# Kernel optimization log

Measured on AMD Instinct MI355X. Metric: run time of the kernel, lower is better.

Reference implementation:

```python
import jax, jax.numpy as jnp
import numpy as np

EPS = 1e-5
H = 96  # spatial size (scaled from 256 to fit memory budget)


def _conv3x3(x, w):
    return jax.lax.conv_general_dilated(x, w, (1, 1), ((1, 1), (1, 1)),
                                        dimension_numbers=('NCHW', 'OIHW', 'NCHW'))


def _conv1x1(x, w, b=None):
    y = jax.lax.conv_general_dilated(x, w, (1, 1), 'VALID',
                                     dimension_numbers=('NCHW', 'OIHW', 'NCHW'))
    if b is not None:
        y = y + b[None, :, None, None]
    return y


def _ln(x, w, b):
    # LayerNorm over (C,H,W) with per-element affine, torch semantics
    m = jnp.mean(x, axis=(1, 2, 3), keepdims=True)
    v = jnp.mean(jnp.square(x - m), axis=(1, 2, 3), keepdims=True)
    return (x - m) * jax.lax.rsqrt(v + EPS) * w[None] + b[None]


def setup_inputs() -> dict:
    key = jax.random.key(0)
    ks = iter(jax.random.split(key, 32))
    s = 0.05
    d = {}
    d['x'] = jax.random.normal(next(ks), (1, 237, H, H), dtype=jnp.float32)
    d['conv1_w'] = jax.random.normal(next(ks), (96, 237, 3, 3), jnp.float32) * s
    d['ln1_w'] = jnp.ones((96, H, H), jnp.float32)
    d['ln1_b'] = jnp.zeros((96, H, H), jnp.float32)
    d['conv2_w'] = jax.random.normal(next(ks), (48, 96, 3, 3), jnp.float32) * s
    d['ln2_w'] = jnp.ones((48, H, H), jnp.float32)
    d['ln2_b'] = jnp.zeros((48, H, H), jnp.float32)
    d['conv3_w'] = jax.random.normal(next(ks), (48, 48, 3, 3), jnp.float32) * s
    d['ln3_w'] = jnp.ones((48, H, H), jnp.float32)
    d['ln3_b'] = jnp.zeros((48, H, H), jnp.float32)
    d['conv4_w'] = jax.random.normal(next(ks), (17, 48, 3, 3), jnp.float32) * s
    d['ln4_w'] = jnp.ones((17, H, H), jnp.float32)
    d['ln4_b'] = jnp.zeros((17, H, H), jnp.float32)
    d['cam_gamma'] = jax.random.normal(next(ks), (1,), jnp.float32) * 0.1
    # PAM (dim_reduse=1 -> 17->17 q/k/v 1x1 convs, bias=True)
    d['q_w'] = jax.random.normal(next(ks), (17, 17, 1, 1), jnp.float32) * s
    d['q_b'] = jnp.zeros((17,), jnp.float32)
    d['k_w'] = jax.random.normal(next(ks), (17, 17, 1, 1), jnp.float32) * s
    d['k_b'] = jnp.zeros((17,), jnp.float32)
    d['v_w'] = jax.random.normal(next(ks), (17, 17, 1, 1), jnp.float32) * s
    d['v_b'] = jnp.zeros((17,), jnp.float32)
    d['pam_gamma'] = jax.random.normal(next(ks), (1,), jnp.float32) * 0.1
    d['conv5_w'] = jax.random.normal(next(ks), (17, 17, 1, 1), jnp.float32) * s
    d['ln5_w'] = jnp.ones((17, H, H), jnp.float32)
    d['ln5_b'] = jnp.zeros((17, H, H), jnp.float32)
    d['conv6_w'] = jax.random.normal(next(ks), (17, 17, 1, 1), jnp.float32) * s
    return d


def reference(x, conv1_w, ln1_w, ln1_b, conv2_w, ln2_w, ln2_b,
              conv3_w, ln3_w, ln3_b, conv4_w, ln4_w, ln4_b,
              cam_gamma, q_w, q_b, k_w, k_b, v_w, v_b, pam_gamma,
              conv5_w, ln5_w, ln5_b, conv6_w):
    # backbone: (conv3x3 -> LN -> ReLU) x4
    h = jax.nn.relu(_ln(_conv3x3(x, conv1_w), ln1_w, ln1_b))
    h = jax.nn.relu(_ln(_conv3x3(h, conv2_w), ln2_w, ln2_b))
    h = jax.nn.relu(_ln(_conv3x3(h, conv3_w), ln3_w, ln3_b))
    h = jax.nn.relu(_ln(_conv3x3(h, conv4_w), ln4_w, ln4_b))

    B, C, Hh, Ww = h.shape
    N = Hh * Ww
    hf = h.reshape(B, C, N)

    # CAM: channel attention, [B,C,C]
    e = jnp.einsum('bcn,bdn->bcd', hf, hf)
    e_new = jnp.max(e, axis=-1, keepdims=True) - e
    a_c = jax.nn.softmax(e_new, axis=-1)
    cam = (a_c @ hf).reshape(B, C, Hh, Ww) * cam_gamma

    # PAM: position attention, [B,N,N] (the huge memory-bound matrix)
    q = _conv1x1(h, q_w, q_b).reshape(B, -1, N)   # [B,Cq,N]
    k = _conv1x1(h, k_w, k_b).reshape(B, -1, N)   # [B,Cq,N]
    v = _conv1x1(h, v_w, v_b).reshape(B, C, N)    # [B,C,N]
    energy = jnp.einsum('bcn,bcm->bnm', q, k)      # [B,N,N]
    a_p = jax.nn.softmax(energy, axis=-1)
    pam = jnp.einsum('bcm,bnm->bcn', v, a_p).reshape(B, C, Hh, Ww) * pam_gamma

    y = cam + pam + h
    y = jax.nn.relu(_ln(_conv1x1(y, conv5_w), ln5_w, ln5_b))
    y = _conv1x1(y, conv6_w)
    return y
```

## Files before the change

kernel.cpp:

```cpp
#include <hip/hip_runtime.h>
#include <math.h>

#define HH 96
#define NPIX 9216
#define KSPLIT 32
#define KEYS_PER_SPLIT 288
#define TK 96


__global__ __launch_bounds__(64) void zero_stats_kernel(float* stats) {
    if (threadIdx.x < 16) stats[threadIdx.x] = 0.f;
}

__global__ __launch_bounds__(256) void conv3x3_kernel(
        const float* __restrict__ in, const float* __restrict__ w,
        float* __restrict__ out, int Cin, int Cout) {
    extern __shared__ float smem[];
    float* wl   = smem;
    float* tile = smem + 4 * Cin * 9;

    const int tx = threadIdx.x, ty = threadIdx.y;
    const int tid = ty * 16 + tx;
    const int x0 = blockIdx.x * 16, y0 = blockIdx.y * 16;
    const int co_base = blockIdx.z * 4;
    const int nco = min(4, Cout - co_base);
    const int wcount = nco * Cin * 9;

    for (int i = tid; i < wcount; i += 256)
        wl[i] = w[co_base * Cin * 9 + i];

    float acc[4] = {0.f, 0.f, 0.f, 0.f};

    for (int ci = 0; ci < Cin; ++ci) {
        __syncthreads();
        for (int i = tid; i < 324; i += 256) {
            int r = i / 18, c = i - r * 18;
            int gy = y0 + r - 1, gx = x0 + c - 1;
            float v = 0.f;
            if (gy >= 0 && gy < HH && gx >= 0 && gx < HH)
                v = in[ci * NPIX + gy * HH + gx];
            tile[i] = v;
        }
        __syncthreads();

        float v[9];
        #pragma unroll
        for (int dy = 0; dy < 3; ++dy)
            #pragma unroll
            for (int dx = 0; dx < 3; ++dx)
                v[dy * 3 + dx] = tile[(ty + dy) * 18 + tx + dx];

        #pragma unroll
        for (int j = 0; j < 4; ++j) {
            const float* wp = wl + j * Cin * 9 + ci * 9;
            float a = acc[j];
            #pragma unroll
            for (int kk = 0; kk < 9; ++kk) a += wp[kk] * v[kk];
            acc[j] = a;
        }
    }

    const int oy = y0 + ty, ox = x0 + tx;
    #pragma unroll
    for (int j = 0; j < 4; ++j)
        if (j < nco)
            out[(co_base + j) * NPIX + oy * HH + ox] = acc[j];
}

__global__ __launch_bounds__(256) void ln_reduce_kernel(
        const float* __restrict__ x, int n, float* stats) {
    float s = 0.f, s2 = 0.f;
    for (int i = blockIdx.x * 256 + threadIdx.x; i < n; i += gridDim.x * 256) {
        float v = x[i];
        s += v; s2 += v * v;
    }
    #pragma unroll
    for (int off = 32; off > 0; off >>= 1) {
        s  += __shfl_down(s,  off);
        s2 += __shfl_down(s2, off);
    }
    __shared__ float ls[4], ls2[4];
    int wid = threadIdx.x >> 6;
    if ((threadIdx.x & 63) == 0) { ls[wid] = s; ls2[wid] = s2; }
    __syncthreads();
    if (threadIdx.x == 0) {
        float a = ls[0] + ls[1] + ls[2] + ls[3];
        float b = ls2[0] + ls2[1] + ls2[2] + ls2[3];
        atomicAdd(&stats[0], a);
        atomicAdd(&stats[1], b);
    }
}

__global__ __launch_bounds__(256) void ln_apply_relu_kernel(
        float* __restrict__ x, const float* __restrict__ w,
        const float* __restrict__ b, const float* __restrict__ stats,
        int n, float inv_n) {
    int i = blockIdx.x * 256 + threadIdx.x;
    if (i >= n) return;
    float m   = stats[0] * inv_n;
    float var = stats[1] * inv_n - m * m;
    float inv = rsqrtf(var + 1e-5f);
    float t = (x[i] - m) * inv * w[i] + b[i];
    x[i] = t > 0.f ? t : 0.f;
}

__global__ __launch_bounds__(256) void qkv_kernel(
        const float* __restrict__ h,
        const float* __restrict__ qw, const float* __restrict__ qb,
        const float* __restrict__ kw, const float* __restrict__ kb,
        const float* __restrict__ vw, const float* __restrict__ vb,
        float* __restrict__ q, float* __restrict__ k, float* __restrict__ v) {
    int n = blockIdx.x * 256 + threadIdx.x;
    if (n >= NPIX) return;
    float hv[17];
    #pragma unroll
    for (int c = 0; c < 17; ++c) hv[c] = h[c * NPIX + n];
    #pragma unroll
    for (int co = 0; co < 17; ++co) {
        float sq = qb[co], sk = kb[co], sv = vb[co];
        #pragma unroll
        for (int ci = 0; ci < 17; ++ci) {
            float hh = hv[ci];
            sq += qw[co * 17 + ci] * hh;
            sk += kw[co * 17 + ci] * hh;
            sv += vw[co * 17 + ci] * hh;
        }
        q[co * NPIX + n] = sq;
        k[co * NPIX + n] = sk;
        v[co * NPIX + n] = sv;
    }
}

__global__ __launch_bounds__(256) void cam_e_kernel(const float* __restrict__ h, float* e) {
    int c = blockIdx.x / 17, d = blockIdx.x - c * 17;
    float s = 0.f;
    for (int i = threadIdx.x; i < NPIX; i += 256)
        s += h[c * NPIX + i] * h[d * NPIX + i];
    #pragma unroll
    for (int off = 32; off > 0; off >>= 1) s += __shfl_down(s, off);
    __shared__ float red[4];
    int wid = threadIdx.x >> 6;
    if ((threadIdx.x & 63) == 0) red[wid] = s;
    __syncthreads();
    if (threadIdx.x == 0) e[blockIdx.x] = red[0] + red[1] + red[2] + red[3];
}

__global__ __launch_bounds__(64) void cam_softmax_kernel(const float* __restrict__ e,
                                                         float* __restrict__ a) {
    int c = threadIdx.x;
    if (c >= 17) return;
    float rmax = -1e30f, rmin = 1e30f;
    for (int d = 0; d < 17; ++d) {
        float v = e[c * 17 + d];
        rmax = fmaxf(rmax, v);
        rmin = fminf(rmin, v);
    }
    float mm = rmax - rmin;
    float p[17], sum = 0.f;
    for (int d = 0; d < 17; ++d) {
        p[d] = __expf((rmax - e[c * 17 + d]) - mm);
        sum += p[d];
    }
    float inv = 1.f / sum;
    for (int d = 0; d < 17; ++d) a[c * 17 + d] = p[d] * inv;
}

__global__ __launch_bounds__(256) void pam_flash_kernel(
        const float* __restrict__ q, const float* __restrict__ k,
        const float* __restrict__ v,
        float* __restrict__ m_part, float* __restrict__ l_part,
        float* __restrict__ o_part) {
    __shared__ float kt[17][TK];
    __shared__ float vt[17][TK];
    const int qi = blockIdx.x * 256 + threadIdx.x;
    const int sp = blockIdx.y;
    const int k0 = sp * KEYS_PER_SPLIT;

    float qr[17];
    #pragma unroll
    for (int c = 0; c < 17; ++c) qr[c] = q[c * NPIX + qi];

    float mr = -1e30f, lr = 0.f;
    float orr[17];
    #pragma unroll
    for (int c = 0; c < 17; ++c) orr[c] = 0.f;

    for (int t = 0; t < KEYS_PER_SPLIT / TK; ++t) {
        __syncthreads();
        for (int i = threadIdx.x; i < 17 * TK; i += 256) {
            int c = i / TK, mi = i - c * TK;
            kt[c][mi] = k[c * NPIX + k0 + t * TK + mi];
            vt[c][mi] = v[c * NPIX + k0 + t * TK + mi];
        }
        __syncthreads();
        for (int mm = 0; mm < TK; ++mm) {
            float s0 = 0.f, s1 = 0.f;
            #pragma unroll
            for (int c = 0; c < 16; c += 2) {
                s0 += qr[c]     * kt[c][mm];
                s1 += qr[c + 1] * kt[c + 1][mm];
            }
            float s = s0 + s1 + qr[16] * kt[16][mm];
            if (s > mr + 8.f) {
                float sc = __expf(mr - s);
                lr *= sc;
                #pragma unroll
                for (int c = 0; c < 17; ++c) orr[c] *= sc;
                mr = s;
            }
            float p = __expf(s - mr);
            lr += p;
            #pragma unroll
            for (int c = 0; c < 17; ++c) orr[c] += p * vt[c][mm];
        }
    }

    m_part[sp * NPIX + qi] = mr;
    l_part[sp * NPIX + qi] = lr;
    #pragma unroll
    for (int c = 0; c < 17; ++c)
        o_part[(sp * 17 + c) * NPIX + qi] = orr[c];
}

__global__ __launch_bounds__(256) void pam_merge_kernel(
        const float* __restrict__ m_part, const float* __restrict__ l_part,
        const float* __restrict__ o_part, const float* __restrict__ gamma,
        float* __restrict__ pam) {
    const int qi = blockIdx.x * 256 + threadIdx.x;
    float M = -1e30f;
    #pragma unroll
    for (int s = 0; s < KSPLIT; ++s) M = fmaxf(M, m_part[s * NPIX + qi]);
    float wsc[KSPLIT];
    float L = 0.f;
    #pragma unroll
    for (int s = 0; s < KSPLIT; ++s) {
        float wv = __expf(m_part[s * NPIX + qi] - M);
        wsc[s] = wv;
        L += wv * l_part[s * NPIX + qi];
    }
    float invL = gamma[0] / L;
    for (int c = 0; c < 17; ++c) {
        float acc = 0.f;
        #pragma unroll
        for (int s = 0; s < KSPLIT; ++s)
            acc += wsc[s] * o_part[(s * 17 + c) * NPIX + qi];
        pam[c * NPIX + qi] = acc * invL;
    }
}

__global__ __launch_bounds__(256) void y_combine_kernel(
        const float* __restrict__ h, const float* __restrict__ a,
        const float* __restrict__ cam_gamma, const float* __restrict__ pam,
        float* __restrict__ y) {
    int idx = blockIdx.x * 256 + threadIdx.x;
    if (idx >= 17 * NPIX) return;
    int c = idx / NPIX, n = idx - c * NPIX;
    float s = 0.f;
    #pragma unroll
    for (int d = 0; d < 17; ++d) s += a[c * 17 + d] * h[d * NPIX + n];
    y[idx] = cam_gamma[0] * s + pam[idx] + h[idx];
}

__global__ __launch_bounds__(256) void conv1x1_17_kernel(
        const float* __restrict__ in, const float* __restrict__ w,
        float* __restrict__ out) {
    int idx = blockIdx.x * 256 + threadIdx.x;
    if (idx >= 17 * NPIX) return;
    int c = idx / NPIX, n = idx - c * NPIX;
    float s = 0.f;
    #pragma unroll
    for (int ci = 0; ci < 17; ++ci) s += w[c * 17 + ci] * in[ci * NPIX + n];
    out[idx] = s;
}


extern "C" void kernel_launch(void* const* d_in, const int* in_sizes, int n_in,
                              void* d_out, int out_size, void* d_ws, size_t ws_size,
                              hipStream_t stream) {
    const float* x       = (const float*)d_in[0];
    const float* conv1_w = (const float*)d_in[1];
    const float* ln1_w   = (const float*)d_in[2];
    const float* ln1_b   = (const float*)d_in[3];
    const float* conv2_w = (const float*)d_in[4];
    const float* ln2_w   = (const float*)d_in[5];
    const float* ln2_b   = (const float*)d_in[6];
    const float* conv3_w = (const float*)d_in[7];
    const float* ln3_w   = (const float*)d_in[8];
    const float* ln3_b   = (const float*)d_in[9];
    const float* conv4_w = (const float*)d_in[10];
    const float* ln4_w   = (const float*)d_in[11];
    const float* ln4_b   = (const float*)d_in[12];
    const float* cam_g   = (const float*)d_in[13];
    const float* q_w     = (const float*)d_in[14];
    const float* q_b     = (const float*)d_in[15];
    const float* k_w     = (const float*)d_in[16];
    const float* k_b     = (const float*)d_in[17];
    const float* v_w     = (const float*)d_in[18];
    const float* v_b     = (const float*)d_in[19];
    const float* pam_g   = (const float*)d_in[20];
    const float* conv5_w = (const float*)d_in[21];
    const float* ln5_w   = (const float*)d_in[22];
    const float* ln5_b   = (const float*)d_in[23];
    const float* conv6_w = (const float*)d_in[24];
    float* out = (float*)d_out;

    float* W = (float*)d_ws;
    float* stats  = W;
    float* h1     = W + 16;
    float* h2     = h1 + 96 * NPIX;
    float* h3     = h2 + 48 * NPIX;
    float* h4     = h3 + 48 * NPIX;
    float* qbuf   = h4 + 17 * NPIX;
    float* kbuf   = qbuf + 17 * NPIX;
    float* vbuf   = kbuf + 17 * NPIX;
    float* ebuf   = vbuf + 17 * NPIX;
    float* abuf   = ebuf + 289;
    float* m_part = abuf + 289;
    float* l_part = m_part + KSPLIT * NPIX;
    float* o_part = l_part + KSPLIT * NPIX;
    float* pam    = o_part + KSPLIT * 17 * NPIX;
    float* ybuf   = pam + 17 * NPIX;
    float* t5     = ybuf + 17 * NPIX;

    dim3 b256(256), b16x16(16, 16);

    zero_stats_kernel<<<1, 64, 0, stream>>>(stats);

    {
        size_t lds = (4 * 237 * 9 + 324) * sizeof(float);
        conv3x3_kernel<<<dim3(6, 6, 24), b16x16, lds, stream>>>(x, conv1_w, h1, 237, 96);
        int n = 96 * NPIX;
        ln_reduce_kernel<<<256, b256, 0, stream>>>(h1, n, stats + 0);
        ln_apply_relu_kernel<<<(n + 255) / 256, b256, 0, stream>>>(h1, ln1_w, ln1_b, stats + 0, n, 1.f / n);
    }
    {
        size_t lds = (4 * 96 * 9 + 324) * sizeof(float);
        conv3x3_kernel<<<dim3(6, 6, 12), b16x16, lds, stream>>>(h1, conv2_w, h2, 96, 48);
        int n = 48 * NPIX;
        ln_reduce_kernel<<<256, b256, 0, stream>>>(h2, n, stats + 2);
        ln_apply_relu_kernel<<<(n + 255) / 256, b256, 0, stream>>>(h2, ln2_w, ln2_b, stats + 2, n, 1.f / n);
    }
    {
        size_t lds = (4 * 48 * 9 + 324) * sizeof(float);
        conv3x3_kernel<<<dim3(6, 6, 12), b16x16, lds, stream>>>(h2, conv3_w, h3, 48, 48);
        int n = 48 * NPIX;
        ln_reduce_kernel<<<256, b256, 0, stream>>>(h3, n, stats + 4);
        ln_apply_relu_kernel<<<(n + 255) / 256, b256, 0, stream>>>(h3, ln3_w, ln3_b, stats + 4, n, 1.f / n);
    }
    {
        size_t lds = (4 * 48 * 9 + 324) * sizeof(float);
        conv3x3_kernel<<<dim3(6, 6, 5), b16x16, lds, stream>>>(h3, conv4_w, h4, 48, 17);
        int n = 17 * NPIX;
        ln_reduce_kernel<<<256, b256, 0, stream>>>(h4, n, stats + 6);
        ln_apply_relu_kernel<<<(n + 255) / 256, b256, 0, stream>>>(h4, ln4_w, ln4_b, stats + 6, n, 1.f / n);
    }

    qkv_kernel<<<36, b256, 0, stream>>>(h4, q_w, q_b, k_w, k_b, v_w, v_b, qbuf, kbuf, vbuf);

    cam_e_kernel<<<289, b256, 0, stream>>>(h4, ebuf);
    cam_softmax_kernel<<<1, 64, 0, stream>>>(ebuf, abuf);

    pam_flash_kernel<<<dim3(36, KSPLIT), b256, 0, stream>>>(qbuf, kbuf, vbuf, m_part, l_part, o_part);
    pam_merge_kernel<<<36, b256, 0, stream>>>(m_part, l_part, o_part, pam_g, pam);

    y_combine_kernel<<<(17 * NPIX + 255) / 256, b256, 0, stream>>>(h4, abuf, cam_g, pam, ybuf);
    conv1x1_17_kernel<<<(17 * NPIX + 255) / 256, b256, 0, stream>>>(ybuf, conv5_w, t5);
    {
        int n = 17 * NPIX;
        ln_reduce_kernel<<<256, b256, 0, stream>>>(t5, n, stats + 8);
        ln_apply_relu_kernel<<<(n + 255) / 256, b256, 0, stream>>>(t5, ln5_w, ln5_b, stats + 8, n, 1.f / n);
    }
    conv1x1_17_kernel<<<(17 * NPIX + 255) / 256, b256, 0, stream>>>(t5, conv6_w, out);
}
```

Baseline: 903.7 us.

## Rewrite conv, LN, PAM and tail kernels with fusion and transposed K/V layout

Replaces the conv3x3 kernel with a templated version that computes two pixels per thread, stages 8 input channels per tile and fuses the LayerNorm sum/sumsq reduction into the conv epilogue, which removes the separate reduce passes. The LN apply and CAM dot product are vectorised with float4. PAM now reads K and V in a pixel-major padded layout straight from global memory instead of staging them through LDS, and it uses a different key-split count. The merge kernel is split across channel groups, and the combine, conv5, LN5 and conv6 tail is fused into two kernels. These changes cut launches and memory passes, at the cost of conv weights read from global memory each iteration and more register pressure.

```diff
diff --git a/kernel.cpp b/kernel.cpp
--- a/kernel.cpp
+++ b/kernel.cpp
@@ -1,107 +1,119 @@
 #include <hip/hip_runtime.h>
 #include <math.h>
 
+#define NPIX 9216
 #define HH 96
-#define NPIX 9216
-#define KSPLIT 32
-#define KEYS_PER_SPLIT 288
-#define TK 96
+#define KSPLIT 24
+#define KEYS 384
 
 
 __global__ __launch_bounds__(64) void zero_stats_kernel(float* stats) {
     if (threadIdx.x < 16) stats[threadIdx.x] = 0.f;
 }
 
-__global__ __launch_bounds__(256) void conv3x3_kernel(
-        const float* __restrict__ in, const float* __restrict__ w,
-        float* __restrict__ out, int Cin, int Cout) {
-    extern __shared__ float smem[];
-    float* wl   = smem;
-    float* tile = smem + 4 * Cin * 9;
-
-    const int tx = threadIdx.x, ty = threadIdx.y;
-    const int tid = ty * 16 + tx;
-    const int x0 = blockIdx.x * 16, y0 = blockIdx.y * 16;
-    const int co_base = blockIdx.z * 4;
-    const int nco = min(4, Cout - co_base);
-    const int wcount = nco * Cin * 9;
-
-    for (int i = tid; i < wcount; i += 256)
-        wl[i] = w[co_base * Cin * 9 + i];
-
-    float acc[4] = {0.f, 0.f, 0.f, 0.f};
-
-    for (int ci = 0; ci < Cin; ++ci) {
-        __syncthreads();
-        for (int i = tid; i < 324; i += 256) {
-            int r = i / 18, c = i - r * 18;
-            int gy = y0 + r - 1, gx = x0 + c - 1;
-            float v = 0.f;
-            if (gy >= 0 && gy < HH && gx >= 0 && gx < HH)
-                v = in[ci * NPIX + gy * HH + gx];
-            tile[i] = v;
-        }
-        __syncthreads();
-
-        float v[9];
-        #pragma unroll
-        for (int dy = 0; dy < 3; ++dy)
-            #pragma unroll
-            for (int dx = 0; dx < 3; ++dx)
-                v[dy * 3 + dx] = tile[(ty + dy) * 18 + tx + dx];
-
-        #pragma unroll
-        for (int j = 0; j < 4; ++j) {
-            const float* wp = wl + j * Cin * 9 + ci * 9;
-            float a = acc[j];
-            #pragma unroll
-            for (int kk = 0; kk < 9; ++kk) a += wp[kk] * v[kk];
-            acc[j] = a;
-        }
-    }
-
-    const int oy = y0 + ty, ox = x0 + tx;
-    #pragma unroll
-    for (int j = 0; j < 4; ++j)
-        if (j < nco)
-            out[(co_base + j) * NPIX + oy * HH + ox] = acc[j];
-}
-
-__global__ __launch_bounds__(256) void ln_reduce_kernel(
-        const float* __restrict__ x, int n, float* stats) {
-    float s = 0.f, s2 = 0.f;
-    for (int i = blockIdx.x * 256 + threadIdx.x; i < n; i += gridDim.x * 256) {
-        float v = x[i];
-        s += v; s2 += v * v;
-    }
+__device__ __forceinline__ void wave_stats_atomic(float s, float s2, float* stats, int tid) {
     #pragma unroll
     for (int off = 32; off > 0; off >>= 1) {
         s  += __shfl_down(s,  off);
         s2 += __shfl_down(s2, off);
     }
-    __shared__ float ls[4], ls2[4];
-    int wid = threadIdx.x >> 6;
-    if ((threadIdx.x & 63) == 0) { ls[wid] = s; ls2[wid] = s2; }
-    __syncthreads();
-    if (threadIdx.x == 0) {
-        float a = ls[0] + ls[1] + ls[2] + ls[3];
-        float b = ls2[0] + ls2[1] + ls2[2] + ls2[3];
-        atomicAdd(&stats[0], a);
-        atomicAdd(&stats[1], b);
-    }
+    if ((tid & 63) == 0) {
+        atomicAdd(&stats[0], s);
+        atomicAdd(&stats[1], s2);
+    }
+}
+
+template<int CIN, int CO>
+__global__ __launch_bounds__(256) void conv3x3_t(
+        const float* __restrict__ in, const float* __restrict__ w,
+        float* __restrict__ out, float* __restrict__ stats) {
+    constexpr int STAGES = (CIN + 7) / 8;
+    __shared__ float tile[8][18][36];
+
+    const int tid = threadIdx.x;
+    const int tx = tid & 15, ty = tid >> 4;
+    const int x0 = blockIdx.x * 32, y0 = blockIdx.y * 16;
+    const int co0 = blockIdx.z * CO;
+
+    float acc[CO][2];
+    #pragma unroll
+    for (int j = 0; j < CO; ++j) { acc[j][0] = 0.f; acc[j][1] = 0.f; }
+
+    for (int st = 0; st < STAGES; ++st) {
+        __syncthreads();
+        for (int i = tid; i < 8 * 18 * 34; i += 256) {
+            int ci  = i / (18 * 34);
+            int rem = i - ci * (18 * 34);
+            int r   = rem / 34;
+            int c   = rem - r * 34;
+            int cig = st * 8 + ci;
+            int gy = y0 + r - 1, gx = x0 + c - 1;
+            float v = 0.f;
+            if (cig < CIN && gy >= 0 && gy < HH && gx >= 0 && gx < HH)
+                v = in[cig * NPIX + gy * HH + gx];
+            tile[ci][r][c] = v;
+        }
+        __syncthreads();
+
+        #pragma unroll
+        for (int ci = 0; ci < 8; ++ci) {
+            int cig = st * 8 + ci;
+            int cw = cig < CIN ? cig : CIN - 1;
+            float tv[3][4];
+            #pragma unroll
+            for (int r = 0; r < 3; ++r) {
+                float2 a = *(const float2*)&tile[ci][ty + r][2 * tx];
+                float2 b = *(const float2*)&tile[ci][ty + r][2 * tx + 2];
+                tv[r][0] = a.x; tv[r][1] = a.y; tv[r][2] = b.x; tv[r][3] = b.y;
+            }
+            #pragma unroll
+            for (int j = 0; j < CO; ++j) {
+                const float* wp = w + ((size_t)(co0 + j) * CIN + cw) * 9;
+                #pragma unroll
+                for (int r = 0; r < 3; ++r) {
+                    #pragma unroll
+                    for (int d = 0; d < 3; ++d) {
+                        float wv = wp[r * 3 + d];
+                        acc[j][0] += wv * tv[r][d];
+                        acc[j][1] += wv * tv[r][d + 1];
+                    }
+                }
+            }
+        }
+    }
+
+    const int oy = y0 + ty, ox = x0 + 2 * tx;
+    float s = 0.f, s2 = 0.f;
+    #pragma unroll
+    for (int j = 0; j < CO; ++j) {
+        #pragma unroll
+        for (int p = 0; p < 2; ++p) {
+            float v = acc[j][p];
+            out[(size_t)(co0 + j) * NPIX + oy * HH + ox + p] = v;
+            s += v; s2 += v * v;
+        }
+    }
+    wave_stats_atomic(s, s2, stats, tid);
 }
 
 __global__ __launch_bounds__(256) void ln_apply_relu_kernel(
         float* __restrict__ x, const float* __restrict__ w,
         const float* __restrict__ b, const float* __restrict__ stats,
-        int n, float inv_n) {
+        int n4, float inv_n) {
     int i = blockIdx.x * 256 + threadIdx.x;
-    if (i >= n) return;
+    if (i >= n4) return;
     float m   = stats[0] * inv_n;
     float var = stats[1] * inv_n - m * m;
     float inv = rsqrtf(var + 1e-5f);
-    float t = (x[i] - m) * inv * w[i] + b[i];
-    x[i] = t > 0.f ? t : 0.f;
+    float4 xv = ((const float4*)x)[i];
+    float4 wv = ((const float4*)w)[i];
+    float4 bv = ((const float4*)b)[i];
+    float4 o;
+    o.x = fmaxf((xv.x - m) * inv * wv.x + bv.x, 0.f);
+    o.y = fmaxf((xv.y - m) * inv * wv.y + bv.y, 0.f);
+    o.z = fmaxf((xv.z - m) * inv * wv.z + bv.z, 0.f);
+    o.w = fmaxf((xv.w - m) * inv * wv.w + bv.w, 0.f);
+    ((float4*)x)[i] = o;
 }
 
 __global__ __launch_bounds__(256) void qkv_kernel(
@@ -109,33 +121,41 @@
         const float* __restrict__ qw, const float* __restrict__ qb,
         const float* __restrict__ kw, const float* __restrict__ kb,
         const float* __restrict__ vw, const float* __restrict__ vb,
-        float* __restrict__ q, float* __restrict__ k, float* __restrict__ v) {
+        float* __restrict__ q, float* __restrict__ kT, float* __restrict__ vT) {
     int n = blockIdx.x * 256 + threadIdx.x;
-    if (n >= NPIX) return;
+    int mode = blockIdx.y;
+    const float* w = mode == 0 ? qw : (mode == 1 ? kw : vw);
+    const float* b = mode == 0 ? qb : (mode == 1 ? kb : vb);
     float hv[17];
     #pragma unroll
     for (int c = 0; c < 17; ++c) hv[c] = h[c * NPIX + n];
+    float o[17];
     #pragma unroll
     for (int co = 0; co < 17; ++co) {
-        float sq = qb[co], sk = kb[co], sv = vb[co];
-        #pragma unroll
-        for (int ci = 0; ci < 17; ++ci) {
-            float hh = hv[ci];
-            sq += qw[co * 17 + ci] * hh;
-            sk += kw[co * 17 + ci] * hh;
-            sv += vw[co * 17 + ci] * hh;
-        }
-        q[co * NPIX + n] = sq;
-        k[co * NPIX + n] = sk;
-        v[co * NPIX + n] = sv;
+        float s = b[co];
+        #pragma unroll
+        for (int ci = 0; ci < 17; ++ci) s += w[co * 17 + ci] * hv[ci];
+        o[co] = s;
+    }
+    if (mode == 0) {
+        #pragma unroll
+        for (int c = 0; c < 17; ++c) q[c * NPIX + n] = o[c];
+    } else {
+        float* dst = (mode == 1 ? kT : vT);
+        #pragma unroll
+        for (int c = 0; c < 17; ++c) dst[n * 20 + c] = o[c];
     }
 }
 
 __global__ __launch_bounds__(256) void cam_e_kernel(const float* __restrict__ h, float* e) {
     int c = blockIdx.x / 17, d = blockIdx.x - c * 17;
+    const float4* hc = (const float4*)(h + c * NPIX);
+    const float4* hd = (const float4*)(h + d * NPIX);
     float s = 0.f;
-    for (int i = threadIdx.x; i < NPIX; i += 256)
-        s += h[c * NPIX + i] * h[d * NPIX + i];
+    for (int i = threadIdx.x; i < NPIX / 4; i += 256) {
+        float4 a = hc[i], b = hd[i];
+        s += a.x * b.x + a.y * b.y + a.z * b.z + a.w * b.w;
+    }
     #pragma unroll
     for (int off = 32; off > 0; off >>= 1) s += __shfl_down(s, off);
     __shared__ float red[4];
@@ -155,10 +175,9 @@
         rmax = fmaxf(rmax, v);
         rmin = fminf(rmin, v);
     }
-    float mm = rmax - rmin;
     float p[17], sum = 0.f;
     for (int d = 0; d < 17; ++d) {
-        p[d] = __expf((rmax - e[c * 17 + d]) - mm);
+        p[d] = __expf(rmin - e[c * 17 + d]);
         sum += p[d];
     }
     float inv = 1.f / sum;
@@ -166,15 +185,13 @@
 }
 
 __global__ __launch_bounds__(256) void pam_flash_kernel(
-        const float* __restrict__ q, const float* __restrict__ k,
-        const float* __restrict__ v,
+        const float* __restrict__ q, const float* __restrict__ kT,
+        const float* __restrict__ vT,
         float* __restrict__ m_part, float* __restrict__ l_part,
         float* __restrict__ o_part) {
-    __shared__ float kt[17][TK];
-    __shared__ float vt[17][TK];
     const int qi = blockIdx.x * 256 + threadIdx.x;
     const int sp = blockIdx.y;
-    const int k0 = sp * KEYS_PER_SPLIT;
+    const int k0 = sp * KEYS;
 
     float qr[17];
     #pragma unroll
@@ -185,41 +202,42 @@
     #pragma unroll
     for (int c = 0; c < 17; ++c) orr[c] = 0.f;
 
-    for (int t = 0; t < KEYS_PER_SPLIT / TK; ++t) {
-        __syncthreads();
-        for (int i = threadIdx.x; i < 17 * TK; i += 256) {
-            int c = i / TK, mi = i - c * TK;
-            kt[c][mi] = k[c * NPIX + k0 + t * TK + mi];
-            vt[c][mi] = v[c * NPIX + k0 + t * TK + mi];
+    #pragma unroll 2
+    for (int mm = 0; mm < KEYS; ++mm) {
+        const float4* kp = (const float4*)(kT + (size_t)(k0 + mm) * 20);
+        float4 ka = kp[0], kb = kp[1], kc = kp[2], kd = kp[3];
+        float k16 = kT[(size_t)(k0 + mm) * 20 + 16];
+        float s0 = qr[0] * ka.x + qr[1] * ka.y + qr[2] * ka.z + qr[3] * ka.w;
+        float s1 = qr[4] * kb.x + qr[5] * kb.y + qr[6] * kb.z + qr[7] * kb.w;
+        float s2 = qr[8] * kc.x + qr[9] * kc.y + qr[10] * kc.z + qr[11] * kc.w;
+        float s3 = qr[12] * kd.x + qr[13] * kd.y + qr[14] * kd.z + qr[15] * kd.w;
+        float s = (s0 + s1) + (s2 + s3) + qr[16] * k16;
+
+        if (s > mr + 8.f) {
+            float sc = __expf(mr - s);
+            lr *= sc;
+            #pragma unroll
+            for (int c = 0; c < 17; ++c) orr[c] *= sc;
+            mr = s;
         }
-        __syncthreads();
-        for (int mm = 0; mm < TK; ++mm) {
-            float s0 = 0.f, s1 = 0.f;
-            #pragma unroll
-            for (int c = 0; c < 16; c += 2) {
-                s0 += qr[c]     * kt[c][mm];
-                s1 += qr[c + 1] * kt[c + 1][mm];
-            }
-            float s = s0 + s1 + qr[16] * kt[16][mm];
-            if (s > mr + 8.f) {
-                float sc = __expf(mr - s);
-                lr *= sc;
-                #pragma unroll
-                for (int c = 0; c < 17; ++c) orr[c] *= sc;
-                mr = s;
-            }
-            float p = __expf(s - mr);
-            lr += p;
-            #pragma unroll
-            for (int c = 0; c < 17; ++c) orr[c] += p * vt[c][mm];
-        }
+        float p = __expf(s - mr);
+        lr += p;
+
+        const float4* vp = (const float4*)(vT + (size_t)(k0 + mm) * 20);
+        float4 va = vp[0], vb = vp[1], vc = vp[2], vd = vp[3];
+        float v16 = vT[(size_t)(k0 + mm) * 20 + 16];
+        orr[0]  += p * va.x;  orr[1]  += p * va.y;  orr[2]  += p * va.z;  orr[3]  += p * va.w;
+        orr[4]  += p * vb.x;  orr[5]  += p * vb.y;  orr[6]  += p * vb.z;  orr[7]  += p * vb.w;
+        orr[8]  += p * vc.x;  orr[9]  += p * vc.y;  orr[10] += p * vc.z;  orr[11] += p * vc.w;
+        orr[12] += p * vd.x;  orr[13] += p * vd.y;  orr[14] += p * vd.z;  orr[15] += p * vd.w;
+        orr[16] += p * v16;
     }
 
     m_part[sp * NPIX + qi] = mr;
     l_part[sp * NPIX + qi] = lr;
     #pragma unroll
     for (int c = 0; c < 17; ++c)
-        o_part[(sp * 17 + c) * NPIX + qi] = orr[c];
+        o_part[((size_t)sp * 17 + c) * NPIX + qi] = orr[c];
 }
 
 __global__ __launch_bounds__(256) void pam_merge_kernel(
@@ -227,6 +245,10 @@
         const float* __restrict__ o_part, const float* __restrict__ gamma,
         float* __restrict__ pam) {
     const int qi = blockIdx.x * 256 + threadIdx.x;
+    const int cg = blockIdx.y;
+    const int c_lo = cg * 4;
+    const int c_hi = (cg == 3) ? 17 : c_lo + 4;
+
     float M = -1e30f;
     #pragma unroll
     for (int s = 0; s < KSPLIT; ++s) M = fmaxf(M, m_part[s * NPIX + qi]);
@@ -239,38 +261,65 @@
         L += wv * l_part[s * NPIX + qi];
     }
     float invL = gamma[0] / L;
-    for (int c = 0; c < 17; ++c) {
+    for (int c = c_lo; c < c_hi; ++c) {
         float acc = 0.f;
         #pragma unroll
         for (int s = 0; s < KSPLIT; ++s)
-            acc += wsc[s] * o_part[(s * 17 + c) * NPIX + qi];
+            acc += wsc[s] * o_part[((size_t)s * 17 + c) * NPIX + qi];
         pam[c * NPIX + qi] = acc * invL;
     }
 }
 
-__global__ __launch_bounds__(256) void y_combine_kernel(
+__global__ __launch_bounds__(256) void y_conv5_kernel(
         const float* __restrict__ h, const float* __restrict__ a,
         const float* __restrict__ cam_gamma, const float* __restrict__ pam,
-        float* __restrict__ y) {
-    int idx = blockIdx.x * 256 + threadIdx.x;
-    if (idx >= 17 * NPIX) return;
-    int c = idx / NPIX, n = idx - c * NPIX;
-    float s = 0.f;
-    #pragma unroll
-    for (int d = 0; d < 17; ++d) s += a[c * 17 + d] * h[d * NPIX + n];
-    y[idx] = cam_gamma[0] * s + pam[idx] + h[idx];
-}
-
-__global__ __launch_bounds__(256) void conv1x1_17_kernel(
-        const float* __restrict__ in, const float* __restrict__ w,
-        float* __restrict__ out) {
-    int idx = blockIdx.x * 256 + threadIdx.x;
-    if (idx >= 17 * NPIX) return;
-    int c = idx / NPIX, n = idx - c * NPIX;
-    float s = 0.f;
-    #pragma unroll
-    for (int ci = 0; ci < 17; ++ci) s += w[c * 17 + ci] * in[ci * NPIX + n];
-    out[idx] = s;
+        const float* __restrict__ w5, float* __restrict__ t5,
+        float* __restrict__ stats) {
+    int n = blockIdx.x * 256 + threadIdx.x;
+    float hv[17], yv[17];
+    #pragma unroll
+    for (int c = 0; c < 17; ++c) hv[c] = h[c * NPIX + n];
+    float g = cam_gamma[0];
+    #pragma unroll
+    for (int c = 0; c < 17; ++c) {
+        float s = 0.f;
+        #pragma unroll
+        for (int d = 0; d < 17; ++d) s += a[c * 17 + d] * hv[d];
+        yv[c] = g * s + pam[c * NPIX + n] + hv[c];
+    }
+    float s = 0.f, s2 = 0.f;
+    #pragma unroll
+    for (int co = 0; co < 17; ++co) {
+        float t = 0.f;
+        #pragma unroll
+        for (int ci = 0; ci < 17; ++ci) t += w5[co * 17 + ci] * yv[ci];
+        t5[co * NPIX + n] = t;
+        s += t; s2 += t * t;
+    }
+    wave_stats_atomic(s, s2, stats, threadIdx.x);
+}
+
+__global__ __launch_bounds__(256) void ln5_conv6_kernel(
+        const float* __restrict__ t5, const float* __restrict__ lnw,
+        const float* __restrict__ lnb, const float* __restrict__ stats,
+        const float* __restrict__ w6, float* __restrict__ out, float inv_n) {
+    int n = blockIdx.x * 256 + threadIdx.x;
+    float m   = stats[0] * inv_n;
+    float var = stats[1] * inv_n - m * m;
+    float inv = rsqrtf(var + 1e-5f);
+    float act[17];
+    #pragma unroll
+    for (int c = 0; c < 17; ++c) {
+        float t = (t5[c * NPIX + n] - m) * inv * lnw[c * NPIX + n] + lnb[c * NPIX + n];
+        act[c] = fmaxf(t, 0.f);
+    }
+    #pragma unroll
+    for (int co = 0; co < 17; ++co) {
+        float s = 0.f;
+        #pragma unroll
+        for (int ci = 0; ci < 17; ++ci) s += w6[co * 17 + ci] * act[ci];
+        out[co * NPIX + n] = s;
+    }
 }
 
 
@@ -305,70 +354,61 @@
     float* out = (float*)d_out;
 
     float* W = (float*)d_ws;
-    float* stats  = W;
-    float* h1     = W + 16;
-    float* h2     = h1 + 96 * NPIX;
-    float* h3     = h2 + 48 * NPIX;
-    float* h4     = h3 + 48 * NPIX;
-    float* qbuf   = h4 + 17 * NPIX;
-    float* kbuf   = qbuf + 17 * NPIX;
-    float* vbuf   = kbuf + 17 * NPIX;
-    float* ebuf   = vbuf + 17 * NPIX;
-    float* abuf   = ebuf + 289;
-    float* m_part = abuf + 289;
-    float* l_part = m_part + KSPLIT * NPIX;
-    float* o_part = l_part + KSPLIT * NPIX;
-    float* pam    = o_part + KSPLIT * 17 * NPIX;
-    float* ybuf   = pam + 17 * NPIX;
-    float* t5     = ybuf + 17 * NPIX;
-
-    dim3 b256(256), b16x16(16, 16);
+    size_t cur = 0;
+    auto alloc = [&](size_t nfloats) {
+        float* p = W + cur;
+        cur += (nfloats + 15) & ~(size_t)15;
+        return p;
+    };
+    float* stats  = alloc(16);
+    float* h1     = alloc(96 * NPIX);
+    float* h2     = alloc(48 * NPIX);
+    float* h3     = alloc(48 * NPIX);
+    float* h4     = alloc(17 * NPIX);
+    float* qbuf   = alloc(17 * NPIX);
+    float* kT     = alloc(NPIX * 20);
+    float* vT     = alloc(NPIX * 20);
+    float* ebuf   = alloc(289);
+    float* abuf   = alloc(289);
+    float* m_part = alloc(KSPLIT * NPIX);
+    float* l_part = alloc(KSPLIT * NPIX);
+    float* o_part = alloc((size_t)KSPLIT * 17 * NPIX);
+    float* pam    = alloc(17 * NPIX);
+    float* t5     = alloc(17 * NPIX);
+
+    dim3 b256(256);
 
     zero_stats_kernel<<<1, 64, 0, stream>>>(stats);
 
+    conv3x3_t<237, 4><<<dim3(3, 6, 24), b256, 0, stream>>>(x, conv1_w, h1, stats + 0);
     {
-        size_t lds = (4 * 237 * 9 + 324) * sizeof(float);
-        conv3x3_kernel<<<dim3(6, 6, 24), b16x16, lds, stream>>>(x, conv1_w, h1, 237, 96);
         int n = 96 * NPIX;
-        ln_reduce_kernel<<<256, b256, 0, stream>>>(h1, n, stats + 0);
-        ln_apply_relu_kernel<<<(n + 255) / 256, b256, 0, stream>>>(h1, ln1_w, ln1_b, stats + 0, n, 1.f / n);
-    }
+        ln_apply_relu_kernel<<<(n / 4 + 255) / 256, b256, 0, stream>>>(h1, ln1_w, ln1_b, stats + 0, n / 4, 1.f / n);
+    }
+    conv3x3_t<96, 2><<<dim3(3, 6, 24), b256, 0, stream>>>(h1, conv2_w, h2, stats + 2);
     {
-        size_t lds = (4 * 96 * 9 + 324) * sizeof(float);
-        conv3x3_kernel<<<dim3(6, 6, 12), b16x16, lds, stream>>>(h1, conv2_w, h2, 96, 48);
         int n = 48 * NPIX;
-        ln_reduce_kernel<<<256, b256, 0, stream>>>(h2, n, stats + 2);
-        ln_apply_relu_kernel<<<(n + 255) / 256, b256, 0, stream>>>(h2, ln2_w, ln2_b, stats + 2, n, 1.f / n);
-    }
+        ln_apply_relu_kernel<<<(n / 4 + 255) / 256, b256, 0, stream>>>(h2, ln2_w, ln2_b, stats + 2, n / 4, 1.f / n);
+    }
+    conv3x3_t<48, 2><<<dim3(3, 6, 24), b256, 0, stream>>>(h2, conv3_w, h3, stats + 4);
     {
-        size_t lds = (4 * 48 * 9 + 324) * sizeof(float);
-        conv3x3_kernel<<<dim3(6, 6, 12), b16x16, lds, stream>>>(h2, conv3_w, h3, 48, 48);
         int n = 48 * NPIX;
-        ln_reduce_kernel<<<256, b256, 0, stream>>>(h3, n, stats + 4);
-        ln_apply_relu_kernel<<<(n + 255) / 256, b256, 0, stream>>>(h3, ln3_w, ln3_b, stats + 4, n, 1.f / n);
-    }
+        ln_apply_relu_kernel<<<(n / 4 + 255) / 256, b256, 0, stream>>>(h3, ln3_w, ln3_b, stats + 4, n / 4, 1.f / n);
+    }
+    conv3x3_t<48, 1><<<dim3(3, 6, 17), b256, 0, stream>>>(h3, conv4_w, h4, stats + 6);
     {
-        size_t lds = (4 * 48 * 9 + 324) * sizeof(float);
-        conv3x3_kernel<<<dim3(6, 6, 5), b16x16, lds, stream>>>(h3, conv4_w, h4, 48, 17);
         int n = 17 * NPIX;
-        ln_reduce_kernel<<<256, b256, 0, stream>>>(h4, n, stats + 6);
-        ln_apply_relu_kernel<<<(n + 255) / 256, b256, 0, stream>>>(h4, ln4_w, ln4_b, stats + 6, n, 1.f / n);
-    }
-
-    qkv_kernel<<<36, b256, 0, stream>>>(h4, q_w, q_b, k_w, k_b, v_w, v_b, qbuf, kbuf, vbuf);
+        ln_apply_relu_kernel<<<(n / 4 + 255) / 256, b256, 0, stream>>>(h4, ln4_w, ln4_b, stats + 6, n / 4, 1.f / n);
+    }
+
+    qkv_kernel<<<dim3(36, 3), b256, 0, stream>>>(h4, q_w, q_b, k_w, k_b, v_w, v_b, qbuf, kT, vT);
 
     cam_e_kernel<<<289, b256, 0, stream>>>(h4, ebuf);
     cam_softmax_kernel<<<1, 64, 0, stream>>>(ebuf, abuf);
 
-    pam_flash_kernel<<<dim3(36, KSPLIT), b256, 0, stream>>>(qbuf, kbuf, vbuf, m_part, l_part, o_part);
-    pam_merge_kernel<<<36, b256, 0, stream>>>(m_part, l_part, o_part, pam_g, pam);
-
-    y_combine_kernel<<<(17 * NPIX + 255) / 256, b256, 0, stream>>>(h4, abuf, cam_g, pam, ybuf);
-    conv1x1_17_kernel<<<(17 * NPIX + 255) / 256, b256, 0, stream>>>(ybuf, conv5_w, t5);
-    {
-        int n = 17 * NPIX;
-        ln_reduce_kernel<<<256, b256, 0, stream>>>(t5, n, stats + 8);
-        ln_apply_relu_kernel<<<(n + 255) / 256, b256, 0, stream>>>(t5, ln5_w, ln5_b, stats + 8, n, 1.f / n);
-    }
-    conv1x1_17_kernel<<<(17 * NPIX + 255) / 256, b256, 0, stream>>>(t5, conv6_w, out);
-}
+    pam_flash_kernel<<<dim3(36, KSPLIT), b256, 0, stream>>>(qbuf, kT, vT, m_part, l_part, o_part);
+    pam_merge_kernel<<<dim3(36, 4), b256, 0, stream>>>(m_part, l_part, o_part, pam_g, pam);
+
+    y_conv5_kernel<<<36, b256, 0, stream>>>(h4, abuf, cam_g, pam, conv5_w, t5, stats + 8);
+    ln5_conv6_kernel<<<36, b256, 0, stream>>>(t5, ln5_w, ln5_b, stats + 8, conv6_w, out, 1.f / (17 * NPIX));
+}
```

Measured after the change: 1.035 ms. 14.5% more time.
